# Performance work log

Measured on AMD Instinct MI355X. Metric: run time of the kernel, lower is better.

The kernel has to match this reference:

```python
import jax, jax.numpy as jnp
import numpy as np

B, F, V, E, A = 8192, 39, 1_000_000, 16, 16  # batch, fields, vocab, embed, attn


def setup_inputs() -> dict:
    key = jax.random.key(0)
    ks = jax.random.split(key, 9)
    return {
        "feat_index": jax.random.randint(ks[0], (B, F), 0, V),
        "feat_value": jax.random.uniform(ks[1], (B, F), dtype=jnp.float32),
        "first_order_weights": jax.random.normal(ks[2], (V, 1), dtype=jnp.float32) * 0.01,
        "emb_table": jax.random.normal(ks[3], (V, E), dtype=jnp.float32) * 0.01,
        "bias": jax.random.normal(ks[4], (1,), dtype=jnp.float32),
        "attention_w": jax.random.normal(ks[5], (E, A), dtype=jnp.float32) * 0.1,
        "attention_b": jax.random.normal(ks[6], (A,), dtype=jnp.float32) * 0.1,
        "projection_h": jax.random.normal(ks[7], (A, 1), dtype=jnp.float32) * 0.1,
        "projection_p": jax.random.normal(ks[8], (E, 1), dtype=jnp.float32) * 0.1,
    }


def reference(feat_index, feat_value, first_order_weights, emb_table, bias,
              attention_w, attention_b, projection_h, projection_p):
    fv = feat_value[..., None]                                  # [B,F,1]
    # first order: gather weights, scale by value, sum over fields
    y_first = jnp.sum(first_order_weights[feat_index] * fv, axis=1)[:, 0]  # [B]
    # embeddings scaled by feature values
    emb = emb_table[feat_index] * fv                            # [B,F,E]
    # pairwise bi-interaction over all i<j field pairs (num_pairs = F*(F-1)/2)
    iu, ju = np.triu_indices(F, k=1)
    bi = emb[:, iu, :] * emb[:, ju, :]                          # [B,P,E]
    # tiny attention MLP + softmax over pairs
    att = jax.nn.relu(jnp.einsum('bpe,ea->bpa', bi, attention_w) + attention_b)
    score = jax.nn.softmax(jnp.einsum('bpa,ao->bpo', att, projection_h), axis=1)  # [B,P,1]
    pooled = jnp.sum(score * bi, axis=1)                        # [B,E]
    aw = (pooled @ projection_p)[:, 0]                          # [B]
    y = bias + y_first + aw                                     # [B]
    return jax.nn.sigmoid(y)
```

## Files before the change

### kernel.cpp

```cpp
#include <hip/hip_runtime.h>
#include <math.h>


#define BB 8192
#define FF 39
#define PP 741
#define NT 24
#define RBYTES 48
#define SBYTES (FF * RBYTES)

typedef short bf16x8 __attribute__((ext_vector_type(8)));
typedef float f32x4  __attribute__((ext_vector_type(4)));
typedef float f32x16 __attribute__((ext_vector_type(16)));

static __device__ __forceinline__ unsigned pack2(float lo, float hi) {
    return __builtin_amdgcn_perm(__builtin_bit_cast(unsigned, hi),
                                 __builtin_bit_cast(unsigned, lo),
                                 0x07060302u);
}
static __device__ __forceinline__ float up_lo(unsigned d) {
    return __builtin_bit_cast(float, d << 16);
}
static __device__ __forceinline__ float up_hi(unsigned d) {
    return __builtin_bit_cast(float, d & 0xFFFF0000u);
}

__global__ __launch_bounds__(256)
void afm_kernel(const int*   __restrict__ fidx,
                const float* __restrict__ fval,
                const float* __restrict__ fow,
                const float* __restrict__ emb,
                const float* __restrict__ bias,
                const float* __restrict__ aw_,
                const float* __restrict__ ab_,
                const float* __restrict__ ph_,
                const float* __restrict__ pp_,
                float*       __restrict__ out)
{
    __shared__ __align__(16) unsigned char s_emb[4 * SBYTES];
    __shared__ unsigned s_pij[NT * 32];

    const int tid  = threadIdx.x;
    const int wid  = tid >> 6;
    const int lane = tid & 63;
    const int n    = lane & 31;
    const int h    = lane >> 5;
    const int smp  = blockIdx.x * 4 + wid;

    if (tid < FF - 1) {
        int i = tid;
        int base = (i * (2 * FF - i - 1)) >> 1;
        for (int j = i + 1; j < FF; ++j)
            s_pij[base++] = ((unsigned)(i * RBYTES) << 16) | (unsigned)(j * RBYTES);
    } else if (tid == FF - 1) {
        for (int e = PP; e < NT * 32; ++e) s_pij[e] = 0u;
    }

    int ixr = 0; float vr = 0.f, fo = 0.f;
    if (lane < FF) {
        ixr = fidx[smp * FF + lane];
        vr  = fval[smp * FF + lane];
        fo  = fow[ixr] * vr;
    }
    #pragma unroll
    for (int m = 1; m < 64; m <<= 1) fo += __shfl_xor(fo, m);

    unsigned char* my = s_emb + wid * SBYTES;
    for (int u = lane; u < FF * 2; u += 64) {
        int row = u >> 1, hh = u & 1;
        int   ix = __shfl(ixr, row);
        float v  = __shfl(vr,  row);
        const float4* src = (const float4*)emb + (size_t)ix * 4 + hh * 2;
        float4 e0 = src[0], e1 = src[1];
        uint4 d = make_uint4(pack2(e0.x * v, e0.y * v),
                             pack2(e0.z * v, e0.w * v),
                             pack2(e1.x * v, e1.y * v),
                             pack2(e1.z * v, e1.w * v));
        *(uint4*)(my + row * RBYTES + hh * 16) = d;
    }

    const float LOG2E = 1.44269504088896f;
    f32x4 h_lo = ((const f32x4*)ph_)[h];
    f32x4 h_hi = ((const f32x4*)ph_)[h + 2];
    #pragma unroll
    for (int r = 0; r < 4; ++r) { h_lo[r] *= LOG2E; h_hi[r] *= LOG2E; }

    f32x16 cinit;
    {
        const f32x4 ab_lo = ((const f32x4*)ab_)[h];
        const f32x4 ab_hi = ((const f32x4*)ab_)[h + 2];
        cinit[0] = ab_lo[0]; cinit[1] = ab_lo[1];
        cinit[2] = ab_lo[2]; cinit[3] = ab_lo[3];
        cinit[4] = ab_hi[0]; cinit[5] = ab_hi[1];
        cinit[6] = ab_hi[2]; cinit[7] = ab_hi[3];
        #pragma unroll
        for (int r = 8; r < 16; ++r) cinit[r] = 0.f;
    }

    bf16x8 wfrag;
    {
        float t0 = 0.f, t1 = 0.f, t2 = 0.f, t3 = 0.f,
              t4 = 0.f, t5 = 0.f, t6 = 0.f, t7 = 0.f;
        if (n < 16) {
            const float* base = aw_ + (8 * h) * 16 + n;
            t0 = base[0];   t1 = base[16];  t2 = base[32];  t3 = base[48];
            t4 = base[64];  t5 = base[80];  t6 = base[96];  t7 = base[112];
        }
        union { unsigned i[4]; bf16x8 v; } u;
        u.i[0] = pack2(t0, t1); u.i[1] = pack2(t2, t3);
        u.i[2] = pack2(t4, t5); u.i[3] = pack2(t6, t7);
        wfrag = u.v;
    }

    __syncthreads();

    const unsigned char* bpre = my + h * 16;
    const unsigned* pijp = s_pij + n;
    float p0=0.f,p1=0.f,p2=0.f,p3=0.f,p4=0.f,p5=0.f,p6=0.f,p7=0.f;
    float z = 0.f;

#define TILE(PK, MASKED, MOK)                                             \
    {                                                                     \
        unsigned pk = (PK);                                               \
        uint4 di = *(const uint4*)(bpre + (pk >> 16));                    \
        uint4 dj = *(const uint4*)(bpre + (pk & 0xFFFFu));                \
        float m0 = up_lo(di.x) * up_lo(dj.x);                             \
        float m1 = up_hi(di.x) * up_hi(dj.x);                             \
        float m2 = up_lo(di.y) * up_lo(dj.y);                             \
        float m3 = up_hi(di.y) * up_hi(dj.y);                             \
        float m4 = up_lo(di.z) * up_lo(dj.z);                             \
        float m5 = up_hi(di.z) * up_hi(dj.z);                             \
        float m6 = up_lo(di.w) * up_lo(dj.w);                             \
        float m7 = up_hi(di.w) * up_hi(dj.w);                             \
        union { unsigned i[4]; bf16x8 v; } u;                             \
        u.i[0] = pack2(m0, m1); u.i[1] = pack2(m2, m3);                   \
        u.i[2] = pack2(m4, m5); u.i[3] = pack2(m6, m7);                   \
        f32x16 d = __builtin_amdgcn_mfma_f32_32x32x16_bf16(wfrag, u.v,    \
                                                           cinit, 0, 0, 0); \
        float s = fmaf(fmaxf(d[0], 0.f), h_lo[0],                         \
                  fmaf(fmaxf(d[1], 0.f), h_lo[1],                         \
                  fmaf(fmaxf(d[2], 0.f), h_lo[2],                         \
                  fmaf(fmaxf(d[3], 0.f), h_lo[3],                         \
                  fmaf(fmaxf(d[4], 0.f), h_hi[0],                         \
                  fmaf(fmaxf(d[5], 0.f), h_hi[1],                         \
                  fmaf(fmaxf(d[6], 0.f), h_hi[2],                         \
                       fmaxf(d[7], 0.f) * h_hi[3])))))));                 \
        s += __shfl_xor(s, 32);                                           \
        float w = __builtin_amdgcn_exp2f(s);                              \
        if (MASKED) w = (MOK) ? w : 0.f;                                  \
        z += w;                                                           \
        p0 = fmaf(w, m0, p0); p1 = fmaf(w, m1, p1);                       \
        p2 = fmaf(w, m2, p2); p3 = fmaf(w, m3, p3);                       \
        p4 = fmaf(w, m4, p4); p5 = fmaf(w, m5, p5);                       \
        p6 = fmaf(w, m6, p6); p7 = fmaf(w, m7, p7);                       \
    }

    #pragma unroll 4
    for (int t = 0; t < NT - 1; ++t)
        TILE(pijp[t * 32], false, true);
    TILE(pijp[(NT - 1) * 32], true, (n < PP - (NT - 1) * 32));
#undef TILE

    const float4 pf0 = ((const float4*)pp_)[2 * h];
    const float4 pf1 = ((const float4*)pp_)[2 * h + 1];
    float awp = fmaf(p0, pf0.x, fmaf(p1, pf0.y, fmaf(p2, pf0.z,
                fmaf(p3, pf0.w, fmaf(p4, pf1.x, fmaf(p5, pf1.y,
                fmaf(p6, pf1.z, p7 * pf1.w)))))));
    #pragma unroll
    for (int m = 1; m < 64; m <<= 1) {
        awp += __shfl_xor(awp, m);
        z   += __shfl_xor(z, m);
    }
    if (lane == 0) {
        float y = bias[0] + fo + 2.f * awp / z;
        out[smp] = 1.f / (1.f + __expf(-y));
    }
}

extern "C" void kernel_launch(void* const* d_in, const int* in_sizes, int n_in,
                              void* d_out, int out_size, void* d_ws, size_t ws_size,
                              hipStream_t stream) {
    const int*   fidx      = (const int*)  d_in[0];
    const float* fval      = (const float*)d_in[1];
    const float* fow       = (const float*)d_in[2];
    const float* emb_table = (const float*)d_in[3];
    const float* bias      = (const float*)d_in[4];
    const float* attn_w    = (const float*)d_in[5];
    const float* attn_b    = (const float*)d_in[6];
    const float* proj_h    = (const float*)d_in[7];
    const float* proj_p    = (const float*)d_in[8];
    float* out = (float*)d_out;

    afm_kernel<<<BB / 4, 256, 0, stream>>>(fidx, fval, fow, emb_table, bias,
                                           attn_w, attn_b, proj_h, proj_p, out);
}
```

Measured before the change: 132.7 us.

## Split each sample's pair tiles across two wavefronts with LDS reduction

Each sample is now handled by two wavefronts instead of one. The 24 pair tiles are interleaved between them, the gather of embedding rows is split too, and partial sums and softmax denominators are combined through shared memory after a block barrier. The grid doubles and launch bounds ask for 8 blocks per CU. The aim is to shorten each wave's serial MFMA/exp chain and expose more parallelism, at the cost of duplicated index loads, an extra barrier and twice the blocks.

```diff
diff --git a/kernel.cpp b/kernel.cpp
--- a/kernel.cpp
+++ b/kernel.cpp
@@ -6,6 +6,7 @@
 #define FF 39
 #define PP 741
 #define NT 24
+#define NTW 12
 #define RBYTES 48
 #define SBYTES (FF * RBYTES)
 
@@ -25,7 +26,7 @@
     return __builtin_bit_cast(float, d & 0xFFFF0000u);
 }
 
-__global__ __launch_bounds__(256)
+__global__ __launch_bounds__(256, 8)
 void afm_kernel(const int*   __restrict__ fidx,
                 const float* __restrict__ fval,
                 const float* __restrict__ fow,
@@ -37,15 +38,18 @@
                 const float* __restrict__ pp_,
                 float*       __restrict__ out)
 {
-    __shared__ __align__(16) unsigned char s_emb[4 * SBYTES];
+    __shared__ __align__(16) unsigned char s_emb[2 * SBYTES];
     __shared__ unsigned s_pij[NT * 32];
+    __shared__ float s_red[4][2];
 
     const int tid  = threadIdx.x;
     const int wid  = tid >> 6;
     const int lane = tid & 63;
     const int n    = lane & 31;
     const int h    = lane >> 5;
-    const int smp  = blockIdx.x * 4 + wid;
+    const int ws   = wid >> 1;
+    const int wh   = wid & 1;
+    const int smp  = blockIdx.x * 2 + ws;
 
     if (tid < FF - 1) {
         int i = tid;
@@ -60,23 +64,28 @@
     if (lane < FF) {
         ixr = fidx[smp * FF + lane];
         vr  = fval[smp * FF + lane];
-        fo  = fow[ixr] * vr;
-    }
-    #pragma unroll
-    for (int m = 1; m < 64; m <<= 1) fo += __shfl_xor(fo, m);
-
-    unsigned char* my = s_emb + wid * SBYTES;
-    for (int u = lane; u < FF * 2; u += 64) {
-        int row = u >> 1, hh = u & 1;
-        int   ix = __shfl(ixr, row);
-        float v  = __shfl(vr,  row);
-        const float4* src = (const float4*)emb + (size_t)ix * 4 + hh * 2;
-        float4 e0 = src[0], e1 = src[1];
-        uint4 d = make_uint4(pack2(e0.x * v, e0.y * v),
-                             pack2(e0.z * v, e0.w * v),
-                             pack2(e1.x * v, e1.y * v),
-                             pack2(e1.z * v, e1.w * v));
-        *(uint4*)(my + row * RBYTES + hh * 16) = d;
+    }
+    if (wh == 0) {
+        if (lane < FF) fo = fow[ixr] * vr;
+        #pragma unroll
+        for (int m = 1; m < 64; m <<= 1) fo += __shfl_xor(fo, m);
+    }
+
+    unsigned char* my = s_emb + ws * SBYTES;
+    {
+        int u = lane + 64 * wh;
+        if (u < FF * 2) {
+            int row = u >> 1, hh = u & 1;
+            int   ix = __shfl(ixr, row);
+            float v  = __shfl(vr,  row);
+            const float4* src = (const float4*)emb + (size_t)ix * 4 + hh * 2;
+            float4 e0 = src[0], e1 = src[1];
+            uint4 d = make_uint4(pack2(e0.x * v, e0.y * v),
+                                 pack2(e0.z * v, e0.w * v),
+                                 pack2(e1.x * v, e1.y * v),
+                                 pack2(e1.z * v, e1.w * v));
+            *(uint4*)(my + row * RBYTES + hh * 16) = d;
+        }
     }
 
     const float LOG2E = 1.44269504088896f;
@@ -115,51 +124,46 @@
     __syncthreads();
 
     const unsigned char* bpre = my + h * 16;
-    const unsigned* pijp = s_pij + n;
+    const unsigned* pijp = s_pij + wh * 32 + n;
     float p0=0.f,p1=0.f,p2=0.f,p3=0.f,p4=0.f,p5=0.f,p6=0.f,p7=0.f;
     float z = 0.f;
-
-#define TILE(PK, MASKED, MOK)                                             \
-    {                                                                     \
-        unsigned pk = (PK);                                               \
-        uint4 di = *(const uint4*)(bpre + (pk >> 16));                    \
-        uint4 dj = *(const uint4*)(bpre + (pk & 0xFFFFu));                \
-        float m0 = up_lo(di.x) * up_lo(dj.x);                             \
-        float m1 = up_hi(di.x) * up_hi(dj.x);                             \
-        float m2 = up_lo(di.y) * up_lo(dj.y);                             \
-        float m3 = up_hi(di.y) * up_hi(dj.y);                             \
-        float m4 = up_lo(di.z) * up_lo(dj.z);                             \
-        float m5 = up_hi(di.z) * up_hi(dj.z);                             \
-        float m6 = up_lo(di.w) * up_lo(dj.w);                             \
-        float m7 = up_hi(di.w) * up_hi(dj.w);                             \
-        union { unsigned i[4]; bf16x8 v; } u;                             \
-        u.i[0] = pack2(m0, m1); u.i[1] = pack2(m2, m3);                   \
-        u.i[2] = pack2(m4, m5); u.i[3] = pack2(m6, m7);                   \
-        f32x16 d = __builtin_amdgcn_mfma_f32_32x32x16_bf16(wfrag, u.v,    \
-                                                           cinit, 0, 0, 0); \
-        float s = fmaf(fmaxf(d[0], 0.f), h_lo[0],                         \
-                  fmaf(fmaxf(d[1], 0.f), h_lo[1],                         \
-                  fmaf(fmaxf(d[2], 0.f), h_lo[2],                         \
-                  fmaf(fmaxf(d[3], 0.f), h_lo[3],                         \
-                  fmaf(fmaxf(d[4], 0.f), h_hi[0],                         \
-                  fmaf(fmaxf(d[5], 0.f), h_hi[1],                         \
-                  fmaf(fmaxf(d[6], 0.f), h_hi[2],                         \
-                       fmaxf(d[7], 0.f) * h_hi[3])))))));                 \
-        s += __shfl_xor(s, 32);                                           \
-        float w = __builtin_amdgcn_exp2f(s);                              \
-        if (MASKED) w = (MOK) ? w : 0.f;                                  \
-        z += w;                                                           \
-        p0 = fmaf(w, m0, p0); p1 = fmaf(w, m1, p1);                       \
-        p2 = fmaf(w, m2, p2); p3 = fmaf(w, m3, p3);                       \
-        p4 = fmaf(w, m4, p4); p5 = fmaf(w, m5, p5);                       \
-        p6 = fmaf(w, m6, p6); p7 = fmaf(w, m7, p7);                       \
-    }
+    const int lastk = (wh == 1) ? (NTW - 1) : NTW;
 
     #pragma unroll 4
-    for (int t = 0; t < NT - 1; ++t)
-        TILE(pijp[t * 32], false, true);
-    TILE(pijp[(NT - 1) * 32], true, (n < PP - (NT - 1) * 32));
-#undef TILE
+    for (int k = 0; k < NTW; ++k) {
+        unsigned pk = pijp[k * 64];
+        uint4 di = *(const uint4*)(bpre + (pk >> 16));
+        uint4 dj = *(const uint4*)(bpre + (pk & 0xFFFFu));
+        float m0 = up_lo(di.x) * up_lo(dj.x);
+        float m1 = up_hi(di.x) * up_hi(dj.x);
+        float m2 = up_lo(di.y) * up_lo(dj.y);
+        float m3 = up_hi(di.y) * up_hi(dj.y);
+        float m4 = up_lo(di.z) * up_lo(dj.z);
+        float m5 = up_hi(di.z) * up_hi(dj.z);
+        float m6 = up_lo(di.w) * up_lo(dj.w);
+        float m7 = up_hi(di.w) * up_hi(dj.w);
+        union { unsigned i[4]; bf16x8 v; } u;
+        u.i[0] = pack2(m0, m1); u.i[1] = pack2(m2, m3);
+        u.i[2] = pack2(m4, m5); u.i[3] = pack2(m6, m7);
+        f32x16 d = __builtin_amdgcn_mfma_f32_32x32x16_bf16(wfrag, u.v,
+                                                           cinit, 0, 0, 0);
+        float s = fmaf(fmaxf(d[0], 0.f), h_lo[0],
+                  fmaf(fmaxf(d[1], 0.f), h_lo[1],
+                  fmaf(fmaxf(d[2], 0.f), h_lo[2],
+                  fmaf(fmaxf(d[3], 0.f), h_lo[3],
+                  fmaf(fmaxf(d[4], 0.f), h_hi[0],
+                  fmaf(fmaxf(d[5], 0.f), h_hi[1],
+                  fmaf(fmaxf(d[6], 0.f), h_hi[2],
+                       fmaxf(d[7], 0.f) * h_hi[3])))))));
+        s += __shfl_xor(s, 32);
+        float w = __builtin_amdgcn_exp2f(s);
+        if (k == lastk) w = (n < PP - (NT - 1) * 32) ? w : 0.f;
+        z += w;
+        p0 = fmaf(w, m0, p0); p1 = fmaf(w, m1, p1);
+        p2 = fmaf(w, m2, p2); p3 = fmaf(w, m3, p3);
+        p4 = fmaf(w, m4, p4); p5 = fmaf(w, m5, p5);
+        p6 = fmaf(w, m6, p6); p7 = fmaf(w, m7, p7);
+    }
 
     const float4 pf0 = ((const float4*)pp_)[2 * h];
     const float4 pf1 = ((const float4*)pp_)[2 * h + 1];
@@ -171,8 +175,12 @@
         awp += __shfl_xor(awp, m);
         z   += __shfl_xor(z, m);
     }
-    if (lane == 0) {
-        float y = bias[0] + fo + 2.f * awp / z;
+    if (lane == 0) { s_red[wid][0] = awp; s_red[wid][1] = z; }
+    __syncthreads();
+    if (wh == 0 && lane == 0) {
+        float aw = s_red[wid][0] + s_red[wid + 1][0];
+        float zz = s_red[wid][1] + s_red[wid + 1][1];
+        float y = bias[0] + fo + 2.f * aw / zz;
         out[smp] = 1.f / (1.f + __expf(-y));
     }
 }
@@ -191,6 +199,6 @@
     const float* proj_p    = (const float*)d_in[8];
     float* out = (float*)d_out;
 
-    afm_kernel<<<BB / 4, 256, 0, stream>>>(fidx, fval, fow, emb_table, bias,
+    afm_kernel<<<BB / 2, 256, 0, stream>>>(fidx, fval, fow, emb_table, bias,
                                            attn_w, attn_b, proj_h, proj_p, out);
 }
```

Result: slower. 304.7 us (+129.6%).

## Move pair-offset table to device constant memory and drop block barrier

Applied to the files above, without the earlier changes.

Replaces the per-block shared-memory pair-index table, which had to be built at runtime and guarded by __syncthreads, with a compile-time constexpr table in device global memory, laid out so each lane loads its offsets as uint4 vectors. Removing the barrier lets each wave start its own pair loop as soon as its own embeddings are staged, since a wave only reads its own staging region. The tile loop is fully unrolled, the first-order gather is moved after the embedding gather so it overlaps, and launch bounds now request four blocks per multiprocessor. The risks are higher register pressure from full unrolling and offset loads now coming from global memory through cache instead of LDS.

```diff
diff --git a/kernel.cpp b/kernel.cpp
--- a/kernel.cpp
+++ b/kernel.cpp
@@ -13,6 +13,20 @@
 typedef float f32x4  __attribute__((ext_vector_type(4)));
 typedef float f32x16 __attribute__((ext_vector_type(16)));
 
+struct alignas(16) PijT { unsigned v[32][NT]; };
+static constexpr PijT make_pij() {
+    PijT t{};
+    int p = 0;
+    for (int i = 0; i < FF; ++i)
+        for (int j = i + 1; j < FF; ++j) {
+            t.v[p & 31][p >> 5] =
+                ((unsigned)(i * RBYTES) << 16) | (unsigned)(j * RBYTES);
+            ++p;
+        }
+    return t;
+}
+__device__ constexpr PijT c_pij = make_pij();
+
 static __device__ __forceinline__ unsigned pack2(float lo, float hi) {
     return __builtin_amdgcn_perm(__builtin_bit_cast(unsigned, hi),
                                  __builtin_bit_cast(unsigned, lo),
@@ -25,7 +39,7 @@
     return __builtin_bit_cast(float, d & 0xFFFF0000u);
 }
 
-__global__ __launch_bounds__(256)
+__global__ __launch_bounds__(256, 4)
 void afm_kernel(const int*   __restrict__ fidx,
                 const float* __restrict__ fval,
                 const float* __restrict__ fow,
@@ -38,7 +52,6 @@
                 float*       __restrict__ out)
 {
     __shared__ __align__(16) unsigned char s_emb[4 * SBYTES];
-    __shared__ unsigned s_pij[NT * 32];
 
     const int tid  = threadIdx.x;
     const int wid  = tid >> 6;
@@ -47,23 +60,11 @@
     const int h    = lane >> 5;
     const int smp  = blockIdx.x * 4 + wid;
 
-    if (tid < FF - 1) {
-        int i = tid;
-        int base = (i * (2 * FF - i - 1)) >> 1;
-        for (int j = i + 1; j < FF; ++j)
-            s_pij[base++] = ((unsigned)(i * RBYTES) << 16) | (unsigned)(j * RBYTES);
-    } else if (tid == FF - 1) {
-        for (int e = PP; e < NT * 32; ++e) s_pij[e] = 0u;
-    }
-
-    int ixr = 0; float vr = 0.f, fo = 0.f;
+    int ixr = 0; float vr = 0.f;
     if (lane < FF) {
         ixr = fidx[smp * FF + lane];
         vr  = fval[smp * FF + lane];
-        fo  = fow[ixr] * vr;
-    }
-    #pragma unroll
-    for (int m = 1; m < 64; m <<= 1) fo += __shfl_xor(fo, m);
+    }
 
     unsigned char* my = s_emb + wid * SBYTES;
     for (int u = lane; u < FF * 2; u += 64) {
@@ -78,6 +79,10 @@
                              pack2(e1.z * v, e1.w * v));
         *(uint4*)(my + row * RBYTES + hh * 16) = d;
     }
+
+    float fo = (lane < FF) ? fow[ixr] * vr : 0.f;
+    #pragma unroll
+    for (int m = 1; m < 64; m <<= 1) fo += __shfl_xor(fo, m);
 
     const float LOG2E = 1.44269504088896f;
     f32x4 h_lo = ((const f32x4*)ph_)[h];
@@ -112,14 +117,12 @@
         wfrag = u.v;
     }
 
-    __syncthreads();
-
     const unsigned char* bpre = my + h * 16;
-    const unsigned* pijp = s_pij + n;
+    const uint4* myp4 = (const uint4*)c_pij.v[n];
     float p0=0.f,p1=0.f,p2=0.f,p3=0.f,p4=0.f,p5=0.f,p6=0.f,p7=0.f;
     float z = 0.f;
 
-#define TILE(PK, MASKED, MOK)                                             \
+#define TILE(PK, MASKED)                                                  \
     {                                                                     \
         unsigned pk = (PK);                                               \
         uint4 di = *(const uint4*)(bpre + (pk >> 16));                    \
@@ -147,7 +150,7 @@
                        fmaxf(d[7], 0.f) * h_hi[3])))))));                 \
         s += __shfl_xor(s, 32);                                           \
         float w = __builtin_amdgcn_exp2f(s);                              \
-        if (MASKED) w = (MOK) ? w : 0.f;                                  \
+        if (MASKED) w = (n < PP - (NT - 1) * 32) ? w : 0.f;               \
         z += w;                                                           \
         p0 = fmaf(w, m0, p0); p1 = fmaf(w, m1, p1);                       \
         p2 = fmaf(w, m2, p2); p3 = fmaf(w, m3, p3);                       \
@@ -155,10 +158,14 @@
         p6 = fmaf(w, m6, p6); p7 = fmaf(w, m7, p7);                       \
     }
 
-    #pragma unroll 4
-    for (int t = 0; t < NT - 1; ++t)
-        TILE(pijp[t * 32], false, true);
-    TILE(pijp[(NT - 1) * 32], true, (n < PP - (NT - 1) * 32));
+    #pragma unroll
+    for (int g = 0; g < 6; ++g) {
+        uint4 q = myp4[g];
+        TILE(q.x, false);
+        TILE(q.y, false);
+        TILE(q.z, false);
+        TILE(q.w, g == 5);
+    }
 #undef TILE
 
     const float4 pf0 = ((const float4*)pp_)[2 * h];
```

After: 132.3 us. Within noise of the previous version (-0.3%).
